# Kernel tuning notes

Hardware: AMD Instinct MI355X
Metric: run time of the kernel (lower is better)

The kernel has to match this reference:

```python
import jax, jax.numpy as jnp
import numpy as np

B, C, H, W = 4, 256, 32, 32
N_HEADS, N_GROUPS = 8, 4
HEAD_C = C // N_HEADS            # 32
GROUP_C = C // N_GROUPS          # 64
GROUP_HEADS = N_HEADS // N_GROUPS  # 2
OFFSET_RANGE_FACTOR = 4.0
SCALE = HEAD_C ** -0.5
EPS = 1e-5


def grid_sample(img, grid):
    """Bilinear grid_sample, align_corners=True, zeros padding.
    img: (N, Ch, Hi, Wi); grid: (N, Hg, Wg, 2) with (x, y) in [-1, 1]."""
    N, Ch, Hi, Wi = img.shape
    x = (grid[..., 0] + 1.0) * 0.5 * (Wi - 1)
    y = (grid[..., 1] + 1.0) * 0.5 * (Hi - 1)
    x0 = jnp.floor(x); y0 = jnp.floor(y)
    x1 = x0 + 1.0; y1 = y0 + 1.0
    wx1 = x - x0; wx0 = 1.0 - wx1
    wy1 = y - y0; wy0 = 1.0 - wy1
    img_flat = img.reshape(N, Ch, Hi * Wi)

    def corner(xi, yi, w):
        valid = (xi >= 0) & (xi <= Wi - 1) & (yi >= 0) & (yi <= Hi - 1)
        xc = jnp.clip(xi, 0, Wi - 1).astype(jnp.int32)
        yc = jnp.clip(yi, 0, Hi - 1).astype(jnp.int32)
        idx = yc * Wi + xc  # (N, Hg, Wg)
        vals = jax.vmap(lambda im, ix: im[:, ix])(img_flat, idx)  # (N, Ch, Hg, Wg)
        return vals * (w * valid)[:, None, :, :]

    return (corner(x0, y0, wx0 * wy0) + corner(x1, y0, wx1 * wy0)
            + corner(x0, y1, wx0 * wy1) + corner(x1, y1, wx1 * wy1))


def setup_inputs() -> dict:
    key = jax.random.key(0)
    ks = jax.random.split(key, 12)
    s = C ** -0.5
    return {
        "q_feat": jax.random.normal(ks[0], (B, C, H, W), jnp.float32),
        "kv_feat": jax.random.normal(ks[1], (B, C, H, W), jnp.float32),
        "Wq": jax.random.normal(ks[2], (C, C), jnp.float32) * s,
        "bq": jnp.zeros((C,), jnp.float32),
        "Wk": jax.random.normal(ks[3], (C, C), jnp.float32) * s,
        "bk": jnp.zeros((C,), jnp.float32),
        "Wv": jax.random.normal(ks[4], (C, C), jnp.float32) * s,
        "bv": jnp.zeros((C,), jnp.float32),
        "Wo": jax.random.normal(ks[5], (C, C), jnp.float32) * s,
        "bo": jnp.zeros((C,), jnp.float32),
        "off_dw_w": jax.random.normal(ks[6], (GROUP_C, 1, 3, 3), jnp.float32) / 3.0,
        "off_dw_b": jnp.zeros((GROUP_C,), jnp.float32),
        "off_ln_w": jnp.ones((GROUP_C,), jnp.float32),
        "off_ln_b": jnp.zeros((GROUP_C,), jnp.float32),
        "off_pw_w": jax.random.normal(ks[7], (2, GROUP_C), jnp.float32) * GROUP_C ** -0.5,
        "rpe_table": jax.random.normal(ks[8], (N_HEADS, 2 * H - 1, 2 * W - 1), jnp.float32) * 0.01,
    }


def reference(q_feat, kv_feat, Wq, bq, Wk, bk, Wv, bv, Wo, bo,
              off_dw_w, off_dw_b, off_ln_w, off_ln_b, off_pw_w, rpe_table):
    Bg = B * N_GROUPS
    n = H * W
    # q projection (1x1 conv)
    q = jnp.einsum('oi,bihw->bohw', Wq, q_feat) + bq[:, None, None]
    # offset network on grouped q
    q_off = q.reshape(Bg, GROUP_C, H, W)
    x = jax.lax.conv_general_dilated(q_off, off_dw_w, (1, 1), ((1, 1), (1, 1)),
                                     feature_group_count=GROUP_C,
                                     dimension_numbers=('NCHW', 'OIHW', 'NCHW'))
    x = x + off_dw_b[:, None, None]
    mu = x.mean(1, keepdims=True)
    var = x.var(1, keepdims=True)
    x = (x - mu) / jnp.sqrt(var + EPS) * off_ln_w[:, None, None] + off_ln_b[:, None, None]
    x = jax.nn.gelu(x, approximate=False)
    offset = jnp.einsum('oc,bchw->bohw', off_pw_w, x)  # (Bg, 2, H, W), (y, x)
    off_range = jnp.array([1.0 / (H - 1), 1.0 / (W - 1)], jnp.float32).reshape(1, 2, 1, 1)
    offset = jnp.tanh(offset) * off_range * OFFSET_RANGE_FACTOR
    offset = offset.transpose(0, 2, 3, 1)  # (Bg, H, W, 2)
    # reference points in [-1, 1]
    ref_y = (jnp.linspace(0.5, H - 0.5, H) / (H - 1.0)) * 2.0 - 1.0
    ref_x = (jnp.linspace(0.5, W - 0.5, W) / (W - 1.0)) * 2.0 - 1.0
    ref = jnp.stack(jnp.meshgrid(ref_y, ref_x, indexing='ij'), -1)  # (H, W, 2)
    pos = offset + ref[None]  # (Bg, H, W, 2), (y, x), no clamp (offset_range_factor >= 0)
    # deformable sampling of kv features
    kv_g = kv_feat.reshape(Bg, GROUP_C, H, W)
    x_sampled = grid_sample(kv_g, pos[..., ::-1]).reshape(B, C, n)
    k = jnp.einsum('oi,bin->bon', Wk, x_sampled) + bk[:, None]
    v = jnp.einsum('oi,bin->bon', Wv, x_sampled) + bv[:, None]
    qf = q.reshape(B, N_HEADS, HEAD_C, n)
    kf = k.reshape(B, N_HEADS, HEAD_C, n)
    vf = v.reshape(B, N_HEADS, HEAD_C, n)
    attn = jnp.einsum('bhcm,bhcn->bhmn', qf, kf) * SCALE
    # relative-position bias via bilinear sampling of rpe table
    gy = (jnp.arange(H, dtype=jnp.float32) / (H - 1.0)) * 2.0 - 1.0
    gx = (jnp.arange(W, dtype=jnp.float32) / (W - 1.0)) * 2.0 - 1.0
    q_grid = jnp.stack(jnp.meshgrid(gy, gx, indexing='ij'), -1).reshape(n, 2)
    pos_flat = pos.reshape(Bg, n, 2)
    disp = (q_grid[None, :, None, :] - pos_flat[:, None, :, :]) * 0.5  # (Bg, m, n, 2)
    rpe = jnp.broadcast_to(
        rpe_table.reshape(1, N_GROUPS, GROUP_HEADS, 2 * H - 1, 2 * W - 1),
        (B, N_GROUPS, GROUP_HEADS, 2 * H - 1, 2 * W - 1)
    ).reshape(Bg, GROUP_HEADS, 2 * H - 1, 2 * W - 1)
    bias = grid_sample(rpe, disp[..., ::-1])  # (Bg, GROUP_HEADS, m, n)
    attn = attn + bias.reshape(B, N_HEADS, n, n)
    attn = jax.nn.softmax(attn, axis=-1)
    out = jnp.einsum('bhmn,bhcn->bhcm', attn, vf).reshape(B, C, H, W)
    out = jnp.einsum('oi,bihw->bohw', Wo, out) + bo[:, None, None]
    return out
```

## Files before the change

kernel.cpp:

```cpp
#include <hip/hip_runtime.h>
#include <hip/hip_bf16.h>
#include <math.h>

#define BB 4
#define CC 256
#define HH 32
#define WW 32
#define NPIX 1024
#define NHEADS 8
#define NGROUPS 4
#define HEADC 32
#define GROUPC 64
#define BG 16
#define RPE_N 3969
#define SCALE_QK 0.17677669529663687f
#define LN_EPS 1e-5f

#define W_Q   0
#define W_POS 1048576
#define W_XS  1081344
#define W_KT  2129920
#define W_VV  2654208
#define W_AO  3178496

using frag  = __attribute__((ext_vector_type(8))) short;
using f32x4 = __attribute__((ext_vector_type(4))) float;

struct InPtrs { const void* p[16]; };

__device__ __forceinline__ float tof(float x){ return x; }
__device__ __forceinline__ float tof(__hip_bfloat16 x){ return __bfloat162float(x); }
__device__ __forceinline__ short bfs(float v) {
  __hip_bfloat16 h = __float2bfloat16(v);
  return *(short*)&h;
}
__device__ __forceinline__ bool is_f32(const void* lnw) {
  return *(const unsigned int*)lnw == 0x3F800000u;
}
__device__ __forceinline__ float ldm(const void* p, size_t i, bool f32m) {
  return f32m ? ((const float*)p)[i] : __bfloat162float(((const __hip_bfloat16*)p)[i]);
}

template<int TM>
__device__ __forceinline__ void gemm_body(const void* xsrc, bool xf32,
    const void* wraw, bool wf32, int b, int o0, int mb,
    short* Bs, f32x4* acc) {
  const int tid = threadIdx.x;
  const int wave = tid >> 6, lane = tid & 63, quad = lane >> 4, l15 = lane & 15;
  const int og = wave & 3, mh = wave >> 2;
  const int MS = TM >> 5;
  for (int s = 0; s < 8; ++s) {
    const int k0 = s * 32;
    if (s) __syncthreads();
    #pragma unroll
    for (int it = 0; it < (TM >> 4); ++it) {
      int i = tid + 512 * it;
      int mm = i & (TM - 1), kk = i / TM;
      size_t gi = ((size_t)(b * CC + k0 + kk)) * NPIX + mb + mm;
      float v = xf32 ? ((const float*)xsrc)[gi]
                     : __bfloat162float(((const __hip_bfloat16*)xsrc)[gi]);
      __hip_bfloat16 h = __float2bfloat16(v);
      int base = mm * 72 + ((((kk >> 3) ^ (mm & 3))) << 4) + (kk & 7);
      Bs[base] = *(short*)&h;
      Bs[base + 8] = bfs(v - __bfloat162float(h));
    }
    __syncthreads();
    size_t wofs = (size_t)(o0 + og * 16 + l15) * CC + k0 + quad * 8;
    float wv[8];
    if (wf32) {
      float4 wa = *(const float4*)((const float*)wraw + wofs);
      float4 wb = *(const float4*)((const float*)wraw + wofs + 4);
      wv[0]=wa.x; wv[1]=wa.y; wv[2]=wa.z; wv[3]=wa.w;
      wv[4]=wb.x; wv[5]=wb.y; wv[6]=wb.z; wv[7]=wb.w;
    } else {
      const __hip_bfloat16* wp = (const __hip_bfloat16*)wraw + wofs;
      #pragma unroll
      for (int j = 0; j < 8; ++j) wv[j] = __bfloat162float(wp[j]);
    }
    frag wh, wl;
    #pragma unroll
    for (int j = 0; j < 8; ++j) {
      __hip_bfloat16 h = __float2bfloat16(wv[j]);
      wh[j] = *(short*)&h;
      wl[j] = bfs(wv[j] - __bfloat162float(h));
    }
    #pragma unroll
    for (int ms = 0; ms < MS; ++ms) {
      int ml = mh * (TM >> 1) + ms * 16 + l15;
      const short* bp = Bs + ml * 72 + ((quad ^ (ml & 3)) << 4);
      frag bh = *(const frag*)bp;
      frag bl = *(const frag*)(bp + 8);
      acc[ms] = __builtin_amdgcn_mfma_f32_16x16x32_bf16(wh, bh, acc[ms], 0, 0, 0);
      acc[ms] = __builtin_amdgcn_mfma_f32_16x16x32_bf16(wh, bl, acc[ms], 0, 0, 0);
      acc[ms] = __builtin_amdgcn_mfma_f32_16x16x32_bf16(wl, bh, acc[ms], 0, 0, 0);
    }
  }
}

__global__ __launch_bounds__(512)
void qproj_kernel(InPtrs ip, float* __restrict__ q) {
  __shared__ __align__(16) short Bs[32 * 72];
  bool f32m = is_f32(ip.p[12]);
  int mb = blockIdx.x * 32, o0 = blockIdx.y * 64, b = blockIdx.z;
  int tid = threadIdx.x;
  int wave = tid >> 6, lane = tid & 63, quad = lane >> 4, l15 = lane & 15;
  f32x4 acc[1] = {{0.f,0.f,0.f,0.f}};
  gemm_body<32>(ip.p[0], f32m, ip.p[2], f32m, b, o0, mb, Bs, acc);
  int og = wave & 3, mh = wave >> 2;
  int od = o0 + og * 16 + quad * 4;
  float bv[4];
  #pragma unroll
  for (int r = 0; r < 4; ++r) bv[r] = ldm(ip.p[3], od + r, f32m);
  int m = mb + mh * 16 + l15;
  #pragma unroll
  for (int r = 0; r < 4; ++r)
    q[(size_t)(b * CC + od + r) * NPIX + m] = acc[0][r] + bv[r];
}

__global__ __launch_bounds__(512)
void kvproj_kernel(InPtrs ip, const float* __restrict__ xs,
                   __hip_bfloat16* __restrict__ kT, __hip_bfloat16* __restrict__ vbf) {
  __shared__ __align__(16) char arena[16640];
  bool f32m = is_f32(ip.p[12]);
  int mt = blockIdx.x, ot = blockIdx.y, b = blockIdx.z;
  int mb = mt * 64;
  bool isV = (ot >= 4);
  int o0 = (ot & 3) * 64;
  const void* wraw = isV ? ip.p[6] : ip.p[4];
  const void* braw = isV ? ip.p[7] : ip.p[5];
  int tid = threadIdx.x;
  int wave = tid >> 6, lane = tid & 63, quad = lane >> 4, l15 = lane & 15;
  f32x4 acc[2] = {{0.f,0.f,0.f,0.f},{0.f,0.f,0.f,0.f}};
  gemm_body<64>(xs, true, wraw, f32m, b, o0, mb, (short*)arena, acc);
  int og = wave & 3, mh = wave >> 2;
  int od = o0 + og * 16 + quad * 4;
  float bv[4];
  #pragma unroll
  for (int r = 0; r < 4; ++r) bv[r] = ldm(braw, od + r, f32m);
  if (isV) {
    #pragma unroll
    for (int ms = 0; ms < 2; ++ms) {
      int m = mb + mh * 32 + ms * 16 + l15;
      #pragma unroll
      for (int r = 0; r < 4; ++r)
        vbf[(size_t)(b * CC + od + r) * NPIX + m] = __float2bfloat16(acc[ms][r] + bv[r]);
    }
  } else {
    __syncthreads();
    float* Ds = (float*)arena;
    #pragma unroll
    for (int ms = 0; ms < 2; ++ms) {
      int ml = mh * 32 + ms * 16 + l15;
      #pragma unroll
      for (int r = 0; r < 4; ++r)
        Ds[(og * 16 + quad * 4 + r) * 65 + ml] = acc[ms][r] + bv[r];
    }
    __syncthreads();
    int ot4 = ot & 3;
    {
      int q2 = tid;
      int m = q2 >> 3, cc = q2 & 7;
      __hip_bfloat16 t8[8];
      #pragma unroll
      for (int j = 0; j < 8; ++j)
        t8[j] = __float2bfloat16(Ds[(cc * 8 + j) * 65 + m]);
      int h = ot4 * 2 + (cc >> 2);
      size_t addr = ((size_t)(b * NHEADS + h) * NPIX + mb + m) * HEADC + (cc & 3) * 8;
      *(uint4*)((short*)kT + addr) = *(const uint4*)t8;
    }
  }
}

__global__ __launch_bounds__(512)
void oproj_kernel(InPtrs ip, const float* __restrict__ ao, void* __restrict__ out) {
  __shared__ __align__(16) short Bs[32 * 72];
  bool f32m = is_f32(ip.p[12]);
  int mb = blockIdx.x * 32, o0 = blockIdx.y * 64, b = blockIdx.z;
  int tid = threadIdx.x;
  int wave = tid >> 6, lane = tid & 63, quad = lane >> 4, l15 = lane & 15;
  f32x4 acc[1] = {{0.f,0.f,0.f,0.f}};
  gemm_body<32>(ao, true, ip.p[8], f32m, b, o0, mb, Bs, acc);
  int og = wave & 3, mh = wave >> 2;
  int od = o0 + og * 16 + quad * 4;
  float bv[4];
  #pragma unroll
  for (int r = 0; r < 4; ++r) bv[r] = ldm(ip.p[9], od + r, f32m);
  int m = mb + mh * 16 + l15;
  #pragma unroll
  for (int r = 0; r < 4; ++r) {
    float val = acc[0][r] + bv[r];
    size_t idx = (size_t)(b * CC + od + r) * NPIX + m;
    if (f32m) ((float*)out)[idx] = val;
    else      ((__hip_bfloat16*)out)[idx] = __float2bfloat16(val);
  }
}

template<typename T>
__device__ __forceinline__ float tap4(const T* __restrict__ img,
                                      int x0, int y0,
                                      float wx0, float wx1, float wy0, float wy1) {
  bool xv0 = (x0 >= 0) & (x0 < WW);
  bool xv1 = (x0 >= -1) & (x0 < WW - 1);
  bool yv0 = (y0 >= 0) & (y0 < HH);
  bool yv1 = (y0 >= -1) & (y0 < HH - 1);
  float acc = 0.0f;
  if (xv0 & yv0) acc += wx0 * wy0 * tof(img[y0 * WW + x0]);
  if (xv1 & yv0) acc += wx1 * wy0 * tof(img[y0 * WW + x0 + 1]);
  if (xv0 & yv1) acc += wx0 * wy1 * tof(img[(y0 + 1) * WW + x0]);
  if (xv1 & yv1) acc += wx1 * wy1 * tof(img[(y0 + 1) * WW + x0 + 1]);
  return acc;
}

__global__ __launch_bounds__(256)
void offsample_kernel(InPtrs ip, const float* __restrict__ q,
                      float* __restrict__ pos, float* __restrict__ xs) {
  __shared__ float qs[96][65];
  __shared__ float posl[64];
  bool f32m = is_f32(ip.p[12]);
  int blk = blockIdx.x;
  int hh = blk & 31, bg = blk >> 5;
  int b = bg >> 2, g = bg & 3;
  int tid = threadIdx.x;
  const float* qg = q + (size_t)(b * CC + g * GROUPC) * NPIX;
  #pragma unroll
  for (int k = 0; k < 24; ++k) {
    int idx = tid + 256 * k;
    int ww = idx & 31, c = (idx >> 5) & 63, r3 = idx >> 11;
    int yy = hh + r3 - 1;
    float v = (yy >= 0 && yy < HH) ? qg[(size_t)c * NPIX + yy * WW + ww] : 0.0f;
    qs[r3 * 32 + ww][c] = v;
  }
  __syncthreads();
  {
    int wave = tid >> 6, c = tid & 63;
    float wdw[9];
    #pragma unroll
    for (int j = 0; j < 9; ++j) wdw[j] = ldm(ip.p[10], c * 9 + j, f32m);
    float bdw = ldm(ip.p[11], c, f32m);
    float lnw = ldm(ip.p[12], c, f32m), lnb = ldm(ip.p[13], c, f32m);
    float pwy = ldm(ip.p[14], c, f32m), pwx = ldm(ip.p[14], GROUPC + c, f32m);

    for (int p8 = 0; p8 < 8; ++p8) {
      int ww = wave * 8 + p8;
      float x = bdw;
      #pragma unroll
      for (int dy = 0; dy < 3; ++dy)
        #pragma unroll
        for (int dx = 0; dx < 3; ++dx) {
          int xx = ww + dx - 1;
          if (xx >= 0 && xx < WW) x += wdw[dy * 3 + dx] * qs[dy * 32 + xx][c];
        }
      float s = x, s2 = x * x;
      #pragma unroll
      for (int off = 32; off > 0; off >>= 1) {
        s  += __shfl_xor(s,  off);
        s2 += __shfl_xor(s2, off);
      }
      float mu  = s * (1.0f / 64.0f);
      float var = s2 * (1.0f / 64.0f) - mu * mu;
      float xn = (x - mu) * (1.0f / sqrtf(var + LN_EPS)) * lnw + lnb;
      float ge = 0.5f * xn * (1.0f + erff(xn * 0.70710678118654752f));
      float oy = pwy * ge, ox = pwx * ge;
      #pragma unroll
      for (int off = 32; off > 0; off >>= 1) {
        oy += __shfl_xor(oy, off);
        ox += __shfl_xor(ox, off);
      }
      if (c == 0) {
        float fy = tanhf(oy) * (4.0f / 31.0f);
        float fx = tanhf(ox) * (4.0f / 31.0f);
        float ry = ((0.5f + (float)hh) / 31.0f) * 2.0f - 1.0f;
        float rx = ((0.5f + (float)ww) / 31.0f) * 2.0f - 1.0f;
        float py = fy + ry, px = fx + rx;
        int m = hh * 32 + ww;
        pos[((size_t)bg * NPIX + m) * 2 + 0] = py;
        pos[((size_t)bg * NPIX + m) * 2 + 1] = px;
        posl[ww * 2 + 0] = py;
        posl[ww * 2 + 1] = px;
      }
    }
  }
  __syncthreads();
  #pragma unroll
  for (int k = 0; k < 8; ++k) {
    int s = tid + 256 * k;
    int ww = s & 31, c = s >> 5;
    float py = posl[ww * 2 + 0], px = posl[ww * 2 + 1];
    float xi = (px + 1.0f) * 15.5f, yi = (py + 1.0f) * 15.5f;
    float x0f = floorf(xi), y0f = floorf(yi);
    float wx1 = xi - x0f, wx0 = 1.0f - wx1;
    float wy1 = yi - y0f, wy0 = 1.0f - wy1;
    int x0 = (int)x0f, y0 = (int)y0f;
    size_t img_off = (size_t)(b * CC + g * GROUPC + c) * NPIX;
    float acc;
    if (f32m) acc = tap4((const float*)ip.p[1] + img_off, x0, y0, wx0, wx1, wy0, wy1);
    else      acc = tap4((const __hip_bfloat16*)ip.p[1] + img_off, x0, y0, wx0, wx1, wy0, wy1);
    xs[img_off + hh * 32 + ww] = acc;
  }
}

__global__ __launch_bounds__(512)
void attn_mfma_kernel(InPtrs ip, const float* __restrict__ q,
                      const __hip_bfloat16* __restrict__ kT,
                      const __hip_bfloat16* __restrict__ vbf,
                      const float* __restrict__ pos, float* __restrict__ ao) {
  __shared__ __align__(16) __hip_bfloat16 Pl[16][1032];
  __shared__ float rpes[RPE_N];
  __shared__ __align__(16) __hip_bfloat16 qA[2][16][40];
  __shared__ float redmax[8 * 16];
  __shared__ float redsum[8 * 16];

  bool f32m = is_f32(ip.p[12]);
  int bh = blockIdx.x;
  int b = bh >> 3, h = bh & 7;
  int m0base = blockIdx.y * 32;
  int tid = threadIdx.x;
  int bg = b * 4 + (h >> 1);

  size_t slice = (size_t)(b * CC + h * HEADC) * NPIX;
  const short* kTb = (const short*)kT + (size_t)bh * NPIX * HEADC;
  const short* vb = (const short*)vbf + slice;
  const float* qb = q + slice;
  const float* posb = pos + (size_t)bg * NPIX * 2;

  for (int i = tid; i < RPE_N; i += 512)
    rpes[i] = ldm(ip.p[15], (size_t)h * RPE_N + i, f32m);
  {
    int t = tid >> 8, tt = tid & 255;
    int r = tt & 15, c = tt >> 4;
    qA[t][r][c]      = __float2bfloat16(qb[(size_t)c * NPIX + m0base + t * 16 + r] * SCALE_QK);
    qA[t][r][c + 16] = __float2bfloat16(qb[(size_t)(c + 16) * NPIX + m0base + t * 16 + r] * SCALE_QK);
  }
  __syncthreads();

  int wave = tid >> 6, lane = tid & 63;
  int quad = lane >> 4, l15 = lane & 15;
  int nbase = wave * 128;
  float qgy = (float)(m0base >> 5) * (2.0f / 31.0f) - 1.0f;
  float ybase = 31.0f + 15.5f * qgy;

  for (int t = 0; t < 2; ++t) {
    int m0 = m0base + t * 16;
    if (t) __syncthreads();

    frag aq = *(const frag*)&qA[t][l15][quad * 8];
    float qgx0 = (float)(m0 & 31) * (2.0f / 31.0f) - 1.0f;
    float xbase0 = 31.0f + 15.5f * qgx0;

    float sreg[8][4];
    #pragma unroll
    for (int t8 = 0; t8 < 8; ++t8) {
      int n = nbase + t8 * 16 + l15;
      frag bk = *(const frag*)(kTb + (size_t)n * HEADC + quad * 8);
      f32x4 d = __builtin_amdgcn_mfma_f32_16x16x32_bf16(aq, bk, (f32x4){0.f,0.f,0.f,0.f}, 0, 0, 0);
      float2 pp = *(const float2*)(posb + 2 * n);
      float yi = ybase - 15.5f * pp.x;
      float y0f = floorf(yi);
      int y0 = (int)y0f;
      float wy1 = yi - y0f, wy0 = 1.0f - wy1;
      bool yv0 = (y0 >= 0) & (y0 < 63);
      bool yv1 = (y0 >= -1) & (y0 < 62);
      int row0 = y0 * 63;
      float xi0 = xbase0 - 15.5f * pp.y;
      float x0f = floorf(xi0);
      int x0 = (int)x0f;
      float wx1 = xi0 - x0f, wx0 = 1.0f - wx1;
      float u[5];
      #pragma unroll
      for (int jj = 0; jj < 5; ++jj) {
        int xj = x0 + quad * 4 + jj;
        bool xv = (xj >= 0) & (xj < 63);
        int a = row0 + xj;
        int a0c = min(max(a, 0), RPE_N - 1);
        int a1c = min(max(a + 63, 0), RPE_N - 1);
        float t0 = (yv0 & xv) ? rpes[a0c] : 0.0f;
        float t1 = (yv1 & xv) ? rpes[a1c] : 0.0f;
        u[jj] = wy0 * t0 + wy1 * t1;
      }
      #pragma unroll
      for (int reg = 0; reg < 4; ++reg)
        sreg[t8][reg] = d[reg] + wx0 * u[reg] + wx1 * u[reg + 1];
    }

    float ps[4], pm[4];
    #pragma unroll
    for (int reg = 0; reg < 4; ++reg) {
      float m = sreg[0][reg];
      #pragma unroll
      for (int t8 = 1; t8 < 8; ++t8) m = fmaxf(m, sreg[t8][reg]);
      m = fmaxf(m, __shfl_xor(m, 1));
      m = fmaxf(m, __shfl_xor(m, 2));
      m = fmaxf(m, __shfl_xor(m, 4));
      m = fmaxf(m, __shfl_xor(m, 8));
      pm[reg] = m;
      ps[reg] = 0.0f;
    }
    #pragma unroll
    for (int t8 = 0; t8 < 8; ++t8) {
      int n = nbase + t8 * 16 + l15;
      #pragma unroll
      for (int reg = 0; reg < 4; ++reg) {
        float p = __expf(sreg[t8][reg] - pm[reg]);
        Pl[quad * 4 + reg][n] = __float2bfloat16(p);
        ps[reg] += p;
      }
    }
    #pragma unroll
    for (int reg = 0; reg < 4; ++reg) {
      ps[reg] += __shfl_xor(ps[reg], 1);
      ps[reg] += __shfl_xor(ps[reg], 2);
      ps[reg] += __shfl_xor(ps[reg], 4);
      ps[reg] += __shfl_xor(ps[reg], 8);
    }
    if (l15 == 0) {
      #pragma unroll
      for (int reg = 0; reg < 4; ++reg) {
        redmax[wave * 16 + quad * 4 + reg] = pm[reg];
        redsum[wave * 16 + quad * 4 + reg] = ps[reg];
      }
    }

    f32x4 acc0 = {0.f,0.f,0.f,0.f}, acc1 = {0.f,0.f,0.f,0.f};
    #pragma unroll
    for (int ks = 0; ks < 4; ++ks) {
      int koff = nbase + ks * 32 + quad * 8;
      frag ap = *(const frag*)&Pl[l15][koff];
      frag bv0 = *(const frag*)(vb + (size_t)l15 * NPIX + koff);
      frag bv1 = *(const frag*)(vb + (size_t)(16 + l15) * NPIX + koff);
      acc0 = __builtin_amdgcn_mfma_f32_16x16x32_bf16(ap, bv0, acc0, 0, 0, 0);
      acc1 = __builtin_amdgcn_mfma_f32_16x16x32_bf16(ap, bv1, acc1, 0, 0, 0);
    }
    __syncthreads();

    float* part = (float*)&Pl[0][0];
    {
      int e0 = (0 * 16 + l15) * 16 + quad * 4;
      int e1 = (1 * 16 + l15) * 16 + quad * 4;
      #pragma unroll
      for (int reg = 0; reg < 4; ++reg) {
        part[wave * 512 + e0 + reg] = acc0[reg];
        part[wave * 512 + e1 + reg] = acc1[reg];
      }
    }
    __syncthreads();

    {
      int c = tid >> 4, r = tid & 15;
      float M = -1e30f;
      #pragma unroll
      for (int w2 = 0; w2 < 8; ++w2) M = fmaxf(M, redmax[w2 * 16 + r]);
      float num = 0.0f, den = 0.0f;
      #pragma unroll
      for (int w2 = 0; w2 < 8; ++w2) {
        float sc = __expf(redmax[w2 * 16 + r] - M);
        num += part[w2 * 512 + tid] * sc;
        den += redsum[w2 * 16 + r] * sc;
      }
      ao[slice + (size_t)c * NPIX + m0 + r] = num / den;
    }
  }
}

extern "C" void kernel_launch(void* const* d_in, const int* in_sizes, int n_in,
                              void* d_out, int out_size, void* d_ws, size_t ws_size,
                              hipStream_t stream) {
  float* ws  = (float*)d_ws;
  float* q   = ws + W_Q;
  float* pos = ws + W_POS;
  float* xs  = ws + W_XS;
  __hip_bfloat16* kT  = (__hip_bfloat16*)(ws + W_KT);
  __hip_bfloat16* vbf = (__hip_bfloat16*)(ws + W_VV);
  float* ao  = ws + W_AO;

  InPtrs ip;
  for (int i = 0; i < 16; ++i) ip.p[i] = d_in[i];

  qproj_kernel<<<dim3(32, 4, 4), 512, 0, stream>>>(ip, q);
  offsample_kernel<<<BG * 32, 256, 0, stream>>>(ip, q, pos, xs);
  kvproj_kernel<<<dim3(16, 8, 4), 512, 0, stream>>>(ip, xs, kT, vbf);
  attn_mfma_kernel<<<dim3(32, 32), 512, 0, stream>>>(ip, q, kT, vbf, pos, ao);
  oproj_kernel<<<dim3(32, 4, 4), 512, 0, stream>>>(ip, ao, d_out);
}
```

Measured before the change: 216.9 us.

## Double-buffer LDS activation tiles with register prefetch in projection GEMMs

The shared GEMM body now keeps two LDS buffers for the activation tile. Each k-slice's global loads are issued into registers one iteration ahead, so they overlap with the weight conversion and MFMA work of the current slice. This cuts the barriers per k-step from two to one and hides global load latency in the Q, KV and output projection kernels. In exchange it doubles the LDS footprint of those kernels and uses more registers for the prefetched values and precomputed addresses.

Result: faster. 204.3 us (-5.8%).

```diff
diff --git a/kernel.cpp b/kernel.cpp
--- a/kernel.cpp
+++ b/kernel.cpp
@@ -49,22 +49,40 @@
   const int wave = tid >> 6, lane = tid & 63, quad = lane >> 4, l15 = lane & 15;
   const int og = wave & 3, mh = wave >> 2;
   const int MS = TM >> 5;
+  const int NE = TM >> 4;
+
+  size_t gbase[NE];
+  int lbase[NE];
+  #pragma unroll
+  for (int it = 0; it < NE; ++it) {
+    int i = tid + 512 * it;
+    int mm = i & (TM - 1), kk = i / TM;
+    gbase[it] = ((size_t)(b * CC + kk)) * NPIX + mb + mm;
+    lbase[it] = mm * 72 + ((((kk >> 3) ^ (mm & 3))) << 4) + (kk & 7);
+  }
+
+  float v[NE];
+  #pragma unroll
+  for (int it = 0; it < NE; ++it)
+    v[it] = xf32 ? ((const float*)xsrc)[gbase[it]]
+                 : __bfloat162float(((const __hip_bfloat16*)xsrc)[gbase[it]]);
+
   for (int s = 0; s < 8; ++s) {
+    short* buf = Bs + (s & 1) * (TM * 72);
+    #pragma unroll
+    for (int it = 0; it < NE; ++it) {
+      __hip_bfloat16 h = __float2bfloat16(v[it]);
+      buf[lbase[it]] = *(short*)&h;
+      buf[lbase[it] + 8] = bfs(v[it] - __bfloat162float(h));
+    }
+    if (s < 7) {
+      size_t koff = (size_t)(s + 1) * 32 * NPIX;
+      #pragma unroll
+      for (int it = 0; it < NE; ++it)
+        v[it] = xf32 ? ((const float*)xsrc)[gbase[it] + koff]
+                     : __bfloat162float(((const __hip_bfloat16*)xsrc)[gbase[it] + koff]);
+    }
     const int k0 = s * 32;
-    if (s) __syncthreads();
-    #pragma unroll
-    for (int it = 0; it < (TM >> 4); ++it) {
-      int i = tid + 512 * it;
-      int mm = i & (TM - 1), kk = i / TM;
-      size_t gi = ((size_t)(b * CC + k0 + kk)) * NPIX + mb + mm;
-      float v = xf32 ? ((const float*)xsrc)[gi]
-                     : __bfloat162float(((const __hip_bfloat16*)xsrc)[gi]);
-      __hip_bfloat16 h = __float2bfloat16(v);
-      int base = mm * 72 + ((((kk >> 3) ^ (mm & 3))) << 4) + (kk & 7);
-      Bs[base] = *(short*)&h;
-      Bs[base + 8] = bfs(v - __bfloat162float(h));
-    }
-    __syncthreads();
     size_t wofs = (size_t)(o0 + og * 16 + l15) * CC + k0 + quad * 8;
     float wv[8];
     if (wf32) {
@@ -84,10 +102,11 @@
       wh[j] = *(short*)&h;
       wl[j] = bfs(wv[j] - __bfloat162float(h));
     }
+    __syncthreads();
     #pragma unroll
     for (int ms = 0; ms < MS; ++ms) {
       int ml = mh * (TM >> 1) + ms * 16 + l15;
-      const short* bp = Bs + ml * 72 + ((quad ^ (ml & 3)) << 4);
+      const short* bp = buf + ml * 72 + ((quad ^ (ml & 3)) << 4);
       frag bh = *(const frag*)bp;
       frag bl = *(const frag*)(bp + 8);
       acc[ms] = __builtin_amdgcn_mfma_f32_16x16x32_bf16(wh, bh, acc[ms], 0, 0, 0);
@@ -99,7 +118,7 @@
 
 __global__ __launch_bounds__(512)
 void qproj_kernel(InPtrs ip, float* __restrict__ q) {
-  __shared__ __align__(16) short Bs[32 * 72];
+  __shared__ __align__(16) short Bs[2 * 32 * 72];
   bool f32m = is_f32(ip.p[12]);
   int mb = blockIdx.x * 32, o0 = blockIdx.y * 64, b = blockIdx.z;
   int tid = threadIdx.x;
@@ -120,7 +139,7 @@
 __global__ __launch_bounds__(512)
 void kvproj_kernel(InPtrs ip, const float* __restrict__ xs,
                    __hip_bfloat16* __restrict__ kT, __hip_bfloat16* __restrict__ vbf) {
-  __shared__ __align__(16) char arena[16640];
+  __shared__ __align__(16) char arena[2 * 64 * 72 * 2];
   bool f32m = is_f32(ip.p[12]);
   int mt = blockIdx.x, ot = blockIdx.y, b = blockIdx.z;
   int mb = mt * 64;
@@ -173,7 +192,7 @@
 
 __global__ __launch_bounds__(512)
 void oproj_kernel(InPtrs ip, const float* __restrict__ ao, void* __restrict__ out) {
-  __shared__ __align__(16) short Bs[32 * 72];
+  __shared__ __align__(16) short Bs[2 * 32 * 72];
   bool f32m = is_f32(ip.p[12]);
   int mb = blockIdx.x * 32, o0 = blockIdx.y * 64, b = blockIdx.z;
   int tid = threadIdx.x;
```
